# Performance work log

Hardware: AMD Instinct MI355X
Metric: run time of the kernel (lower is better)

Reference implementation:

```python
import jax, jax.numpy as jnp
import numpy as np

HEADS = 8
GROUPS = 8
EPS = 1e-5

def setup_inputs() -> dict:
    key = jax.random.key(0)
    ks = jax.random.split(key, 12)
    B, C, S = 2, 256, 16
    x = jax.random.normal(ks[0], (B, C, S, S, S), dtype=jnp.float32)
    std = 1.0 / np.sqrt(C)
    def lin(k):
        kw, kb = jax.random.split(k)
        W = jax.random.uniform(kw, (C, C), jnp.float32, -std, std)
        b = jax.random.uniform(kb, (C,), jnp.float32, -std, std)
        return W, b
    Wq, bq = lin(ks[1])
    Wk, bk = lin(ks[2])
    Wv, bv = lin(ks[3])
    Wo, bo = lin(ks[4])
    gamma = jnp.ones((C,), jnp.float32)
    beta = jnp.zeros((C,), jnp.float32)
    return {"x": x, "gamma": gamma, "beta": beta, "Wq": Wq, "bq": bq,
            "Wk": Wk, "bk": bk, "Wv": Wv, "bv": bv, "Wo": Wo, "bo": bo}

def _group_norm(x, gamma, beta):
    B, C = x.shape[0], x.shape[1]
    xg = x.reshape(B, GROUPS, -1)  # [B, G, (C/G)*D*H*W]
    mu = xg.mean(axis=-1, keepdims=True)
    var = xg.var(axis=-1, keepdims=True)
    xg = (xg - mu) * jax.lax.rsqrt(var + EPS)
    xn = xg.reshape(x.shape)
    return xn * gamma[None, :, None, None, None] + beta[None, :, None, None, None]

def _conv1x1(x, W, b):
    # 1x1x1 Conv3d == channel-mixing linear: [B,C,D,H,W] x [O,C]
    return jnp.einsum('bcdhw,oc->bodhw', x, W) + b[None, :, None, None, None]

def reference(x, gamma, beta, Wq, bq, Wk, bk, Wv, bv, Wo, bo):
    B, C, D, H, W = x.shape
    hd = C // HEADS
    N = D * H * W
    xn = _group_norm(x, gamma, beta)
    Q = _conv1x1(xn, Wq, bq).reshape(B, HEADS, hd, N)
    K = _conv1x1(xn, Wk, bk).reshape(B, HEADS, hd, N)
    V = _conv1x1(xn, Wv, bv).reshape(B, HEADS, hd, N)
    scale = jnp.sqrt(jnp.asarray(hd, x.dtype))
    attn = jnp.einsum('bhdn,bhdm->bhnm', Q, K) / scale
    attn = jax.nn.softmax(attn, axis=-1)
    out = jnp.einsum('bhnm,bhdm->bhdn', attn, V).reshape(B, C, D, H, W)
    out = _conv1x1(out, Wo, bo)
    return x + out
```

## Files before the change

### kernel.cpp

```cpp
#include <hip/hip_runtime.h>

typedef unsigned short us;
typedef unsigned int uns;
typedef __attribute__((ext_vector_type(8))) short short8;
typedef __attribute__((ext_vector_type(4))) float floatx4;
typedef __attribute__((ext_vector_type(16))) float floatx16;
typedef __attribute__((ext_vector_type(4))) uns unsx4;

__device__ __forceinline__ us f2b(float f) {
    union { float f; unsigned u; } x; x.f = f;
    unsigned r = x.u + 0x7fffu + ((x.u >> 16) & 1u);
    return (us)(r >> 16);
}
__device__ __forceinline__ uns fbits(float f) {
    union { float f; unsigned u; } x; x.f = f; return x.u;
}
__device__ __forceinline__ uns pk2(float hi, float lo) {
    return __builtin_amdgcn_perm(fbits(hi) + 0x8000u, fbits(lo) + 0x8000u, 0x07060302u);
}
__device__ __forceinline__ uns pk2t(float hi, float lo) {
    return __builtin_amdgcn_perm(fbits(hi), fbits(lo), 0x07060302u);
}
__device__ __forceinline__ float ex2(float x) {
    return __builtin_amdgcn_exp2f(x);
}

#define C_DIM 256
#define N_DIM 4096
#define CN (C_DIM * N_DIM)
#define CSC (0.17677669529663687f * 1.4426950408889634f)

__global__ __launch_bounds__(256) void k_part_prep(
        const float* __restrict__ x, float* __restrict__ part,
        const float* __restrict__ Wq, const float* __restrict__ Wk,
        const float* __restrict__ Wv, const float* __restrict__ Wo,
        const float* __restrict__ bq, const float* __restrict__ bk,
        const float* __restrict__ bv, const float* __restrict__ bo,
        us* __restrict__ Wb, float* __restrict__ bst) {
    const int t = threadIdx.x;
    if (blockIdx.y == 16) {
        const int xb = blockIdx.x;
#pragma unroll
        for (int e = 0; e < 4; ++e) {
            int id = e * 16384 + xb * 256 + t;
            Wb[id]          = f2b(Wq[id] * CSC);
            Wb[65536 + id]  = f2b(Wk[id]);
            Wb[131072 + id] = f2b(Wv[id]);
            Wb[196608 + id] = f2b(Wo[id]);
        }
        if (xb == 0) {
            bst[t]       = bq[t] * CSC;
            bst[256 + t] = bk[t];
            bst[512 + t] = bv[t];
            bst[768 + t] = bo[t];
        }
        return;
    }
    const int bg = blockIdx.y, sl = blockIdx.x;
    const float* base = x + (size_t)bg * 131072 + (size_t)sl * 2048 + t * 8;
    float4 a = *(const float4*)base;
    float4 b = *(const float4*)(base + 4);
    float s  = a.x + a.y + a.z + a.w + b.x + b.y + b.z + b.w;
    float ss = a.x*a.x + a.y*a.y + a.z*a.z + a.w*a.w
             + b.x*b.x + b.y*b.y + b.z*b.z + b.w*b.w;
    __shared__ float r1[256], r2[256];
    r1[t] = s; r2[t] = ss;
    __syncthreads();
    for (int off = 128; off > 0; off >>= 1) {
        if (t < off) { r1[t] += r1[t + off]; r2[t] += r2[t + off]; }
        __syncthreads();
    }
    if (t == 0) {
        part[(bg * 64 + sl) * 2]     = r1[0];
        part[(bg * 64 + sl) * 2 + 1] = r2[0];
    }
}

__global__ __launch_bounds__(256) void k_gn_normT(const float* __restrict__ x,
                                                  const float* __restrict__ gamma,
                                                  const float* __restrict__ beta,
                                                  const float* __restrict__ part,
                                                  us* __restrict__ XT) {
    const int t = threadIdx.x, g = blockIdx.y, z = blockIdx.z;
    const int bg = z * 8 + g;
    __shared__ float scs[32], offs[32], mv[2];
    if (t < 64) {
        float s  = part[(bg * 64 + t) * 2];
        float ss = part[(bg * 64 + t) * 2 + 1];
#pragma unroll
        for (int off = 1; off < 64; off <<= 1) {
            s  += __shfl_xor(s, off, 64);
            ss += __shfl_xor(ss, off, 64);
        }
        if (t == 0) {
            const float inv = 1.f / 131072.f;
            float mean = s * inv;
            float var  = ss * inv - mean * mean;
            mv[0] = mean; mv[1] = rsqrtf(var + 1e-5f);
        }
    }
    __syncthreads();
    if (t < 32) {
        float sc = mv[1] * gamma[g * 32 + t];
        scs[t]  = sc;
        offs[t] = beta[g * 32 + t] - mv[0] * sc;
    }
    __syncthreads();
    const int n = blockIdx.x * 256 + t;
    const float* xp = x + ((size_t)z * 256 + g * 32) * N_DIM + n;
    us* op = XT + ((size_t)z * N_DIM + n) * 256 + g * 32;
#pragma unroll
    for (int c8 = 0; c8 < 4; ++c8) {
        short8 o;
#pragma unroll
        for (int i = 0; i < 8; ++i) {
            int c = c8 * 8 + i;
            float v = xp[(size_t)c * N_DIM];
            o[i] = (short)f2b(v * scs[c] + offs[c]);
        }
        *(short8*)(op + c8 * 8) = o;
    }
}

__global__ __launch_bounds__(256) void k_qkv(const us* __restrict__ W,
                                             const float* __restrict__ bias,
                                             const us* __restrict__ XT,
                                             us* __restrict__ QT,
                                             us* __restrict__ KTg,
                                             us* __restrict__ Vb) {
    const int t = threadIdx.x;
    const int n0 = blockIdx.x * 64, m0 = blockIdx.y * 64, z = blockIdx.z;
    const int l = t & 63, w = t >> 6, l15 = l & 15, quad = l >> 4;
    const int wm = m0 + (w >> 1) * 32, wn = n0 + (w & 1) * 32;
    const us* Ap = W + (size_t)(wm + l15) * 256 + quad * 8;
    const us* Bp = XT + ((size_t)z * N_DIM + wn + l15) * 256 + quad * 8;

    floatx4 acc[2][2] = {};
#pragma unroll
    for (int k0 = 0; k0 < 256; k0 += 32) {
        short8 a0 = *(const short8*)(Ap + k0);
        short8 a1 = *(const short8*)(Ap + k0 + 16 * 256);
        short8 b0 = *(const short8*)(Bp + k0);
        short8 b1 = *(const short8*)(Bp + k0 + 16 * 256);
        acc[0][0] = __builtin_amdgcn_mfma_f32_16x16x32_bf16(a0, b0, acc[0][0], 0, 0, 0);
        acc[0][1] = __builtin_amdgcn_mfma_f32_16x16x32_bf16(a0, b1, acc[0][1], 0, 0, 0);
        acc[1][0] = __builtin_amdgcn_mfma_f32_16x16x32_bf16(a1, b0, acc[1][0], 0, 0, 0);
        acc[1][1] = __builtin_amdgcn_mfma_f32_16x16x32_bf16(a1, b1, acc[1][1], 0, 0, 0);
    }

    if (blockIdx.y < 8) {
        us* Dst = (blockIdx.y < 4) ? QT : KTg;
        const int h = (wm >> 5) & 7, bh = z * 8 + h;
#pragma unroll
        for (int mt = 0; mt < 2; ++mt) {
            const int d0 = mt * 16 + quad * 4;
            float b0v = bias[wm + mt * 16 + quad * 4 + 0];
            float b1v = bias[wm + mt * 16 + quad * 4 + 1];
            float b2v = bias[wm + mt * 16 + quad * 4 + 2];
            float b3v = bias[wm + mt * 16 + quad * 4 + 3];
#pragma unroll
            for (int nt = 0; nt < 2; ++nt) {
                int col = wn + nt * 16 + l15;
                uint2 pw;
                pw.x = pk2(acc[mt][nt][1] + b1v, acc[mt][nt][0] + b0v);
                pw.y = pk2(acc[mt][nt][3] + b3v, acc[mt][nt][2] + b2v);
                *(uint2*)(Dst + ((size_t)bh * N_DIM + col) * 32 + d0) = pw;
            }
        }
    } else {
#pragma unroll
        for (int mt = 0; mt < 2; ++mt)
#pragma unroll
            for (int nt = 0; nt < 2; ++nt)
#pragma unroll
                for (int r = 0; r < 4; ++r) {
                    int row = wm + mt * 16 + quad * 4 + r;
                    int col = wn + nt * 16 + l15;
                    Vb[((size_t)z * 256 + (row - 512)) * N_DIM + col] =
                        f2b(acc[mt][nt][r] + bias[row]);
                }
    }
}

__device__ __forceinline__ floatx16 mfma32(short8 a, short8 b, floatx16 c) {
    return __builtin_amdgcn_mfma_f32_32x32x16_bf16(a, b, c, 0, 0, 0);
}
__device__ __forceinline__ void mkfrag(const floatx16& s, short8& p1, short8& p2) {
    uns d0 = pk2t(ex2(s[1]),  ex2(s[0]));
    uns d1 = pk2t(ex2(s[3]),  ex2(s[2]));
    uns d2 = pk2t(ex2(s[5]),  ex2(s[4]));
    uns d3 = pk2t(ex2(s[7]),  ex2(s[6]));
    uns d4 = pk2t(ex2(s[9]),  ex2(s[8]));
    uns d5 = pk2t(ex2(s[11]), ex2(s[10]));
    uns d6 = pk2t(ex2(s[13]), ex2(s[12]));
    uns d7 = pk2t(ex2(s[15]), ex2(s[14]));
    asm volatile("v_permlane32_swap_b32 %0, %1" : "+v"(d0), "+v"(d2));
    asm volatile("v_permlane32_swap_b32 %0, %1" : "+v"(d1), "+v"(d3));
    asm volatile("v_permlane32_swap_b32 %0, %1" : "+v"(d4), "+v"(d6));
    asm volatile("v_permlane32_swap_b32 %0, %1" : "+v"(d5), "+v"(d7));
    unsx4 u1 = {d0, d1, d2, d3};
    unsx4 u2 = {d4, d5, d6, d7};
    p1 = __builtin_bit_cast(short8, u1);
    p2 = __builtin_bit_cast(short8, u2);
}

__global__ __launch_bounds__(256, 2) void k_attn(const us* __restrict__ QT,
                                                 const us* __restrict__ KTg,
                                                 const us* __restrict__ Vb,
                                                 us* __restrict__ AOT) {
    __shared__ __attribute__((aligned(16))) us Kb[2][64 * 32];
    __shared__ __attribute__((aligned(16))) us Vl[2][32 * 64];
    const int t = threadIdx.x;
    const int l = t & 63, w = t >> 6, hf = l >> 5, k31 = l & 31;
    const int bh = blockIdx.y, z = bh >> 3, hd = bh & 7;
    const us* KTp = KTg + (size_t)bh * N_DIM * 32;
    const us* Vp  = Vb  + ((size_t)z * 256 + hd * 32) * N_DIM;
    const int q0 = blockIdx.x * 128 + w * 32;

    const us* qb = QT + ((size_t)bh * N_DIM + q0 + k31) * 32 + hf * 8;
    short8 bq1 = *(const short8*)qb;
    short8 bq2 = *(const short8*)(qb + 16);
    short8 ones;
#pragma unroll
    for (int j = 0; j < 8; ++j) ones[j] = (short)0x3F80;

    floatx16 o  = (floatx16)0.0f;
    floatx16 dn = (floatx16)0.0f;

    const int krow = w * 16 + (l >> 2), kslot = l & 3;
    const int kxs  = kslot ^ ((l >> 3) & 3);
    const us* kgs  = KTp + (size_t)krow * 32 + kslot * 8;
    us*       kds  = &Kb[0][0] + krow * 32 + kxs * 8;
    const int vrow = w * 8 + (l >> 3), vslot = l & 7;
    const int vxs  = vslot ^ ((l >> 3) & 7);
    const us* vgs  = Vp + (size_t)vrow * N_DIM + vslot * 8;
    us*       vds  = &Vl[0][0] + vrow * 64 + vxs * 8;

    const int kf = (k31 >> 1) & 3;
    const us* ka0p = &Kb[0][0] + k31 * 32 + ((hf)     ^ kf) * 8;
    const us* ka1p = &Kb[0][0] + k31 * 32 + ((2 + hf) ^ kf) * 8;
    const int vf = k31 & 7;
    const us* vp0 = &Vl[0][0] + k31 * 64 + ((0 + hf) ^ vf) * 8;
    const us* vp1 = &Vl[0][0] + k31 * 64 + ((2 + hf) ^ vf) * 8;
    const us* vp2 = &Vl[0][0] + k31 * 64 + ((4 + hf) ^ vf) * 8;
    const us* vp3 = &Vl[0][0] + k31 * 64 + ((6 + hf) ^ vf) * 8;

    {
        int4 gk = *(const int4*)kgs;
        int4 gv = *(const int4*)vgs;
        *(int4*)kds = gk;
        *(int4*)vds = gv;
    }
    __syncthreads();
    int cur = 0;

    for (int m0 = 0; m0 < N_DIM; m0 += 64) {
        const int mnext = (m0 + 64) & (N_DIM - 1);
        int4 ngk = *(const int4*)(kgs + (size_t)mnext * 32);
        int4 ngv = *(const int4*)(vgs + mnext);

        const int bo = cur * 2048;
        short8 ka0 = *(const short8*)(ka0p + bo);
        short8 ka1 = *(const short8*)(ka1p + bo);
        short8 kb0 = *(const short8*)(ka0p + bo + 1024);
        short8 kb1 = *(const short8*)(ka1p + bo + 1024);
        short8 v0  = *(const short8*)(vp0 + bo);
        short8 v1  = *(const short8*)(vp1 + bo);
        short8 v2  = *(const short8*)(vp2 + bo);
        short8 v3  = *(const short8*)(vp3 + bo);

        floatx16 s0 = (floatx16)0.0f, s1 = (floatx16)0.0f;
        s0 = mfma32(ka0, bq1, s0);
        s0 = mfma32(ka1, bq2, s0);
        s1 = mfma32(kb0, bq1, s1);
        s1 = mfma32(kb1, bq2, s1);

        short8 p1, p2, p3, p4;
        mkfrag(s0, p1, p2);
        mkfrag(s1, p3, p4);

        o  = mfma32(v0, p1, o);   dn = mfma32(ones, p1, dn);
        o  = mfma32(v1, p2, o);   dn = mfma32(ones, p2, dn);
        o  = mfma32(v2, p3, o);   dn = mfma32(ones, p3, dn);
        o  = mfma32(v3, p4, o);   dn = mfma32(ones, p4, dn);

        *(int4*)(kds + (cur ^ 1) * 2048) = ngk;
        *(int4*)(vds + (cur ^ 1) * 2048) = ngv;
        __syncthreads();
        cur ^= 1;
    }

    const float inv = 1.f / dn[0];
    const int q = q0 + k31;
    us* op = AOT + ((size_t)z * N_DIM + q) * 256 + hd * 32 + hf * 4;
#pragma unroll
    for (int g = 0; g < 4; ++g) {
        uint2 u;
        u.x = pk2(o[4 * g + 1] * inv, o[4 * g + 0] * inv);
        u.y = pk2(o[4 * g + 3] * inv, o[4 * g + 2] * inv);
        *(uint2*)(op + 8 * g) = u;
    }
}

__global__ __launch_bounds__(256) void k_out(const us* __restrict__ W,
                                             const float* __restrict__ bias,
                                             const us* __restrict__ AOT,
                                             float* __restrict__ Out,
                                             const float* __restrict__ resid) {
    const int t = threadIdx.x;
    const int n0 = blockIdx.x * 64, m0 = blockIdx.y * 64, z = blockIdx.z;
    const int l = t & 63, w = t >> 6, l15 = l & 15, quad = l >> 4;
    const int wm = m0 + (w >> 1) * 32, wn = n0 + (w & 1) * 32;
    const us* Ap = W + (size_t)(wm + l15) * 256 + quad * 8;
    const us* Bp = AOT + ((size_t)z * N_DIM + wn + l15) * 256 + quad * 8;

    floatx4 acc[2][2] = {};
#pragma unroll
    for (int k0 = 0; k0 < 256; k0 += 32) {
        short8 a0 = *(const short8*)(Ap + k0);
        short8 a1 = *(const short8*)(Ap + k0 + 16 * 256);
        short8 b0 = *(const short8*)(Bp + k0);
        short8 b1 = *(const short8*)(Bp + k0 + 16 * 256);
        acc[0][0] = __builtin_amdgcn_mfma_f32_16x16x32_bf16(a0, b0, acc[0][0], 0, 0, 0);
        acc[0][1] = __builtin_amdgcn_mfma_f32_16x16x32_bf16(a0, b1, acc[0][1], 0, 0, 0);
        acc[1][0] = __builtin_amdgcn_mfma_f32_16x16x32_bf16(a1, b0, acc[1][0], 0, 0, 0);
        acc[1][1] = __builtin_amdgcn_mfma_f32_16x16x32_bf16(a1, b1, acc[1][1], 0, 0, 0);
    }

#pragma unroll
    for (int mt = 0; mt < 2; ++mt)
#pragma unroll
        for (int nt = 0; nt < 2; ++nt)
#pragma unroll
            for (int r = 0; r < 4; ++r) {
                int row = wm + mt * 16 + quad * 4 + r;
                int col = wn + nt * 16 + l15;
                size_t oidx = ((size_t)z * 256 + row) * N_DIM + col;
                Out[oidx] = acc[mt][nt][r] + bias[row] + resid[oidx];
            }
}

extern "C" void kernel_launch(void* const* d_in, const int* in_sizes, int n_in,
                              void* d_out, int out_size, void* d_ws, size_t ws_size,
                              hipStream_t stream) {
    (void)in_sizes; (void)n_in; (void)out_size; (void)ws_size;
    const float* x     = (const float*)d_in[0];
    const float* gamma = (const float*)d_in[1];
    const float* beta  = (const float*)d_in[2];
    const float* Wq = (const float*)d_in[3]; const float* bq = (const float*)d_in[4];
    const float* Wk = (const float*)d_in[5]; const float* bk = (const float*)d_in[6];
    const float* Wv = (const float*)d_in[7]; const float* bv = (const float*)d_in[8];
    const float* Wo = (const float*)d_in[9]; const float* bo = (const float*)d_in[10];

    float* part = (float*)d_ws;
    us*    Wb   = (us*)((char*)d_ws + 16384);
    float* bst  = (float*)((char*)d_ws + 16384 + 524288);
    us*    XT   = (us*)((char*)d_ws + 16384 + 524288 + 4096);
    us*    QT   = XT + 2 * CN;
    us*    AOT  = QT + 2 * CN;
    us*    Vb   = (us*)d_out;
    us*    KTg  = (us*)d_out + 2 * CN;

    k_part_prep<<<dim3(64, 17), dim3(256), 0, stream>>>(x, part, Wq, Wk, Wv, Wo,
                                                        bq, bk, bv, bo, Wb, bst);
    k_gn_normT<<<dim3(16, 8, 2), dim3(256), 0, stream>>>(x, gamma, beta, part, XT);
    k_qkv<<<dim3(64, 12, 2), dim3(256), 0, stream>>>(Wb, bst, XT, QT, KTg, Vb);
    k_attn<<<dim3(32, 16), dim3(256), 0, stream>>>(QT, KTg, Vb, AOT);
    k_out<<<dim3(64, 4, 2), dim3(256), 0, stream>>>(Wb + 196608, bst + 768, AOT,
                                                    (float*)d_out, x);
}
```

Before: 170.4 us.

## Split attention key range across two wave groups with LDS reduction

Doubles the attention block to 512 threads, and each group of four waves processes half of the key/value sequence (split-K). The two partial numerators and denominators are combined through shared memory before normalization and the bf16 store. The aim is more waves in flight for the same 512-block grid, hiding latency and shortening the serial key loop. The cost is a larger LDS footprint, an extra barrier and reduction step, and heavier register pressure under the 512x4 launch bounds.

```diff
diff --git a/kernel.cpp b/kernel.cpp
--- a/kernel.cpp
+++ b/kernel.cpp
@@ -204,18 +204,20 @@
     p2 = __builtin_bit_cast(short8, u2);
 }
 
-__global__ __launch_bounds__(256, 2) void k_attn(const us* __restrict__ QT,
+__global__ __launch_bounds__(512, 4) void k_attn(const us* __restrict__ QT,
                                                  const us* __restrict__ KTg,
                                                  const us* __restrict__ Vb,
                                                  us* __restrict__ AOT) {
-    __shared__ __attribute__((aligned(16))) us Kb[2][64 * 32];
-    __shared__ __attribute__((aligned(16))) us Vl[2][32 * 64];
+    __shared__ __attribute__((aligned(16))) us SM[16384];
+    us* Kbase = SM;
+    us* Vbase = SM + 8192;
     const int t = threadIdx.x;
     const int l = t & 63, w = t >> 6, hf = l >> 5, k31 = l & 31;
+    const int sw = w & 3, kh = w >> 2;
     const int bh = blockIdx.y, z = bh >> 3, hd = bh & 7;
     const us* KTp = KTg + (size_t)bh * N_DIM * 32;
     const us* Vp  = Vb  + ((size_t)z * 256 + hd * 32) * N_DIM;
-    const int q0 = blockIdx.x * 128 + w * 32;
+    const int q0 = blockIdx.x * 128 + sw * 32;
 
     const us* qb = QT + ((size_t)bh * N_DIM + q0 + k31) * 32 + hf * 8;
     short8 bq1 = *(const short8*)qb;
@@ -227,23 +229,23 @@
     floatx16 o  = (floatx16)0.0f;
     floatx16 dn = (floatx16)0.0f;
 
-    const int krow = w * 16 + (l >> 2), kslot = l & 3;
+    const int krow = sw * 16 + (l >> 2), kslot = l & 3;
     const int kxs  = kslot ^ ((l >> 3) & 3);
-    const us* kgs  = KTp + (size_t)krow * 32 + kslot * 8;
-    us*       kds  = &Kb[0][0] + krow * 32 + kxs * 8;
-    const int vrow = w * 8 + (l >> 3), vslot = l & 7;
+    const us* kgs  = KTp + (size_t)(kh * 2048 + krow) * 32 + kslot * 8;
+    us*       kds  = Kbase + kh * 2048 + krow * 32 + kxs * 8;
+    const int vrow = sw * 8 + (l >> 3), vslot = l & 7;
     const int vxs  = vslot ^ ((l >> 3) & 7);
-    const us* vgs  = Vp + (size_t)vrow * N_DIM + vslot * 8;
-    us*       vds  = &Vl[0][0] + vrow * 64 + vxs * 8;
+    const us* vgs  = Vp + (size_t)vrow * N_DIM + kh * 2048 + vslot * 8;
+    us*       vds  = Vbase + kh * 2048 + vrow * 64 + vxs * 8;
 
     const int kf = (k31 >> 1) & 3;
-    const us* ka0p = &Kb[0][0] + k31 * 32 + ((hf)     ^ kf) * 8;
-    const us* ka1p = &Kb[0][0] + k31 * 32 + ((2 + hf) ^ kf) * 8;
+    const us* ka0p = Kbase + kh * 2048 + k31 * 32 + ((hf)     ^ kf) * 8;
+    const us* ka1p = Kbase + kh * 2048 + k31 * 32 + ((2 + hf) ^ kf) * 8;
     const int vf = k31 & 7;
-    const us* vp0 = &Vl[0][0] + k31 * 64 + ((0 + hf) ^ vf) * 8;
-    const us* vp1 = &Vl[0][0] + k31 * 64 + ((2 + hf) ^ vf) * 8;
-    const us* vp2 = &Vl[0][0] + k31 * 64 + ((4 + hf) ^ vf) * 8;
-    const us* vp3 = &Vl[0][0] + k31 * 64 + ((6 + hf) ^ vf) * 8;
+    const us* vp0 = Vbase + kh * 2048 + k31 * 64 + ((0 + hf) ^ vf) * 8;
+    const us* vp1 = Vbase + kh * 2048 + k31 * 64 + ((2 + hf) ^ vf) * 8;
+    const us* vp2 = Vbase + kh * 2048 + k31 * 64 + ((4 + hf) ^ vf) * 8;
+    const us* vp3 = Vbase + kh * 2048 + k31 * 64 + ((6 + hf) ^ vf) * 8;
 
     {
         int4 gk = *(const int4*)kgs;
@@ -254,12 +256,12 @@
     __syncthreads();
     int cur = 0;
 
-    for (int m0 = 0; m0 < N_DIM; m0 += 64) {
-        const int mnext = (m0 + 64) & (N_DIM - 1);
+    for (int m0 = 0; m0 < 2048; m0 += 64) {
+        const int mnext = (m0 + 64) & 2047;
         int4 ngk = *(const int4*)(kgs + (size_t)mnext * 32);
         int4 ngv = *(const int4*)(vgs + mnext);
 
-        const int bo = cur * 2048;
+        const int bo = cur * 4096;
         short8 ka0 = *(const short8*)(ka0p + bo);
         short8 ka1 = *(const short8*)(ka1p + bo);
         short8 kb0 = *(const short8*)(ka0p + bo + 1024);
@@ -284,21 +286,49 @@
         o  = mfma32(v2, p3, o);   dn = mfma32(ones, p3, dn);
         o  = mfma32(v3, p4, o);   dn = mfma32(ones, p4, dn);
 
-        *(int4*)(kds + (cur ^ 1) * 2048) = ngk;
-        *(int4*)(vds + (cur ^ 1) * 2048) = ngv;
+        *(int4*)(kds + (cur ^ 1) * 4096) = ngk;
+        *(int4*)(vds + (cur ^ 1) * 4096) = ngv;
         __syncthreads();
         cur ^= 1;
     }
 
-    const float inv = 1.f / dn[0];
-    const int q = q0 + k31;
-    us* op = AOT + ((size_t)z * N_DIM + q) * 256 + hd * 32 + hf * 4;
-#pragma unroll
-    for (int g = 0; g < 4; ++g) {
-        uint2 u;
-        u.x = pk2(o[4 * g + 1] * inv, o[4 * g + 0] * inv);
-        u.y = pk2(o[4 * g + 3] * inv, o[4 * g + 2] * inv);
-        *(uint2*)(op + 8 * g) = u;
+    float* sc = (float*)SM;
+    if (kh) {
+        float* dst = sc + (size_t)(sw * 64 + l) * 20;
+        *(floatx4*)(dst + 0)  = ((const floatx4*)&o)[0];
+        *(floatx4*)(dst + 4)  = ((const floatx4*)&o)[1];
+        *(floatx4*)(dst + 8)  = ((const floatx4*)&o)[2];
+        *(floatx4*)(dst + 12) = ((const floatx4*)&o)[3];
+        dst[16] = dn[0];
+    }
+    __syncthreads();
+    if (!kh) {
+        const float* src = sc + (size_t)(sw * 64 + l) * 20;
+        floatx4 a0 = *(const floatx4*)(src + 0);
+        floatx4 a1 = *(const floatx4*)(src + 4);
+        floatx4 a2 = *(const floatx4*)(src + 8);
+        floatx4 a3 = *(const floatx4*)(src + 12);
+        const float dtot = dn[0] + src[16];
+
+        float ov[16];
+#pragma unroll
+        for (int i = 0; i < 4; ++i) {
+            ov[i]      = o[i]      + a0[i];
+            ov[4 + i]  = o[4 + i]  + a1[i];
+            ov[8 + i]  = o[8 + i]  + a2[i];
+            ov[12 + i] = o[12 + i] + a3[i];
+        }
+
+        const float inv = 1.f / dtot;
+        const int q = q0 + k31;
+        us* op = AOT + ((size_t)z * N_DIM + q) * 256 + hd * 32 + hf * 4;
+#pragma unroll
+        for (int g = 0; g < 4; ++g) {
+            uint2 u;
+            u.x = pk2(ov[4 * g + 1] * inv, ov[4 * g + 0] * inv);
+            u.y = pk2(ov[4 * g + 3] * inv, ov[4 * g + 2] * inv);
+            *(uint2*)(op + 8 * g) = u;
+        }
     }
 }
 
@@ -365,7 +395,7 @@
                                                         bq, bk, bv, bo, Wb, bst);
     k_gn_normT<<<dim3(16, 8, 2), dim3(256), 0, stream>>>(x, gamma, beta, part, XT);
     k_qkv<<<dim3(64, 12, 2), dim3(256), 0, stream>>>(Wb, bst, XT, QT, KTg, Vb);
-    k_attn<<<dim3(32, 16), dim3(256), 0, stream>>>(QT, KTg, Vb, AOT);
+    k_attn<<<dim3(32, 16), dim3(512), 0, stream>>>(QT, KTg, Vb, AOT);
     k_out<<<dim3(64, 4, 2), dim3(256), 0, stream>>>(Wb + 196608, bst + 768, AOT,
                                                     (float*)d_out, x);
 }
```

Result: no change. 170.0 us (-0.2%).
